# Optimization experiments

Hardware: AMD Instinct MI355X
Metric: run time of the kernel (lower is better)

Reference implementation:

```python
import jax, jax.numpy as jnp
import numpy as np

K = 512       # num_embeddings
D = 64        # dim_embeddings
BETA = 0.25   # commit_gain
GAMMA = 0.99  # EMA decay
EPS = 1e-05   # Laplace smoothing


def setup_inputs() -> dict:
    key = jax.random.key(0)
    k1, k2, k3 = jax.random.split(key, 3)
    enc_pred = jax.random.normal(k1, (32, D, 64, 64), dtype=jnp.float32)
    embeddings = jax.random.normal(k2, (K, D), dtype=jnp.float32)
    ema_m = jax.random.normal(k3, (K, D), dtype=jnp.float32)
    ema_M = jnp.zeros((K, 1), dtype=jnp.float32)
    return {"enc_pred": enc_pred, "embeddings": embeddings,
            "ema_m": ema_m, "ema_M": ema_M}


def reference(enc_pred, embeddings, ema_m, ema_M):
    B, _, H, W = enc_pred.shape
    x = jnp.transpose(enc_pred, (0, 2, 3, 1))          # [B, H, W, D]
    flat = x.reshape(-1, D)                            # [N, D], N = B*H*W

    # Squared L2 distances to all codewords: [N, K]
    dist = (jnp.sum(flat * flat, axis=1, keepdims=True)
            + jnp.sum(embeddings * embeddings, axis=1)
            - 2.0 * flat @ embeddings.T)
    idx = jnp.argmin(dist, axis=1)                     # [N]

    # Codebook lookup (equivalent to one-hot @ embeddings)
    quantized = embeddings[idx].reshape(x.shape)       # [B, H, W, D]

    # EMA codebook update (training branch, no_grad in torch)
    dm = jax.ops.segment_sum(flat, idx, num_segments=K)                 # [K, D]
    counts = jax.ops.segment_sum(jnp.ones((flat.shape[0], 1), flat.dtype),
                                 idx, num_segments=K)                   # [K, 1]
    new_m = GAMMA * ema_m + (1.0 - GAMMA) * dm
    new_M = GAMMA * ema_M + (1.0 - GAMMA) * counts
    N_tot = jnp.sum(new_M)
    new_M = (new_M + EPS) / (N_tot + EPS * K) * N_tot
    new_embeddings = new_m / new_M

    # Commitment loss (quantized detached)
    loss = BETA * jnp.mean((jax.lax.stop_gradient(quantized) - x) ** 2)

    # Straight-through estimator
    quant_ste = x + jax.lax.stop_gradient(quantized - x)
    out = jnp.transpose(quant_ste, (0, 3, 1, 2))       # [B, D, H, W]

    idx_ret = idx.reshape(B, H, W)[:, None, :, :]      # [B, 1, H, W]
    return (out, loss, idx_ret, new_embeddings, new_m, new_M)
```

## Files before the change

### kernel.cpp

```cpp
#include <hip/hip_runtime.h>

#define KCODES 512
#define DIM 64
#define NB 32
#define NH 64
#define NW 64
#define NPTS (NB*NH*NW)
#define HW (NH*NW)

#define O_OUT  0
#define O_LOSS 8388608
#define O_IDX  8388609
#define O_EMB  8519681
#define O_M    8552449
#define O_MM   8585217

#define W_DM   0
#define W_CNT  (KCODES*DIM)
#define W_LOSS (W_CNT + KCODES)
#define W_NEWM (W_LOSS + 1)
#define W_C    (W_NEWM + KCODES)
#define W_TOTAL (W_C + KCODES)

#define XPAD 68
#define EPAD 68

__global__ void cnorm_kernel(const float* __restrict__ emb, float* __restrict__ ws) {
    int k = blockIdx.x * blockDim.x + threadIdx.x;
    if (k >= KCODES) return;
    float s = 0.f;
    #pragma unroll
    for (int d = 0; d < DIM; ++d) { float v = emb[k*DIM + d]; s += v*v; }
    ws[W_C + k] = s;
}

__global__ __launch_bounds__(256, 2) void assign_kernel(
    const float* __restrict__ enc, const float* __restrict__ emb,
    float* __restrict__ out, float* __restrict__ ws)
{
    __shared__ float XL[128*XPAD];
    __shared__ float EL[128*EPAD];
    __shared__ float cnT[128];
    __shared__ int   bestI[128];

    const int t  = threadIdx.x;
    const int tx = t & 15;
    const int ty = t >> 4;
    const int wv = t >> 6, w = t & 63;
    const int R0 = blockIdx.x * 2;

    #pragma unroll
    for (int r2 = 0; r2 < 2; ++r2) {
        int R = R0 + r2, b = R >> 6, h = R & 63;
        const float* base = enc + (size_t)b*64*HW + (size_t)h*64 + w;
        int p = r2*64 + w;
        #pragma unroll
        for (int it = 0; it < 4; ++it) {
            int d0 = (it*4 + wv)*4;
            float4 v = make_float4(base[(size_t)(d0+0)*HW], base[(size_t)(d0+1)*HW],
                                   base[(size_t)(d0+2)*HW], base[(size_t)(d0+3)*HW]);
            *(float4*)(&XL[p*XPAD + d0]) = v;
        }
    }

    float best[8]; int bidx[8];
    #pragma unroll
    for (int i = 0; i < 8; ++i) { best[i] = 3.402823466e38f; bidx[i] = 0; }

    for (int tile = 0; tile < 4; ++tile) {
        __syncthreads();
        const float* esrc = emb + (size_t)tile*128*64;
        #pragma unroll
        for (int it = 0; it < 8; ++it) {
            int idx = t + it*256;
            *(float4*)(&EL[(idx >> 4)*EPAD + (idx & 15)*4]) =
                *(const float4*)(esrc + (idx >> 4)*64 + (idx & 15)*4);
        }
        if (t < 128) cnT[t] = ws[W_C + tile*128 + t];
        __syncthreads();

        float acc[8][8];
        #pragma unroll
        for (int i = 0; i < 8; ++i)
            #pragma unroll
            for (int j = 0; j < 8; ++j) acc[i][j] = 0.f;

        for (int c = 0; c < 16; ++c) {
            float4 xf[8], ef[8];
            #pragma unroll
            for (int i = 0; i < 8; ++i) {
                int p = 2*ty + (i&1) + 32*(i>>1);
                xf[i] = *(const float4*)(&XL[p*XPAD + c*4]);
            }
            #pragma unroll
            for (int j = 0; j < 8; ++j) {
                int r = tx + 16*j;
                ef[j] = *(const float4*)(&EL[r*EPAD + c*4]);
            }
            #pragma unroll
            for (int i = 0; i < 8; ++i)
                #pragma unroll
                for (int j = 0; j < 8; ++j) {
                    acc[i][j] = fmaf(xf[i].x, ef[j].x, acc[i][j]);
                    acc[i][j] = fmaf(xf[i].y, ef[j].y, acc[i][j]);
                    acc[i][j] = fmaf(xf[i].z, ef[j].z, acc[i][j]);
                    acc[i][j] = fmaf(xf[i].w, ef[j].w, acc[i][j]);
                }
        }

        #pragma unroll
        for (int j = 0; j < 8; ++j) {
            int k = tile*128 + tx + 16*j;
            float cn = cnT[tx + 16*j];
            #pragma unroll
            for (int i = 0; i < 8; ++i) {
                float s = cn - 2.f*acc[i][j];
                if (s < best[i] || (s == best[i] && k < bidx[i])) { best[i] = s; bidx[i] = k; }
            }
        }
    }

    #pragma unroll
    for (int i = 0; i < 8; ++i) {
        float b = best[i]; int kx = bidx[i];
        #pragma unroll
        for (int off = 1; off < 16; off <<= 1) {
            float ob = __shfl_xor(b, off, 64);
            int   ok = __shfl_xor(kx, off, 64);
            if (ob < b || (ob == b && ok < kx)) { b = ob; kx = ok; }
        }
        if (tx == 0) bestI[2*ty + (i&1) + 32*(i>>1)] = kx;
    }
    __syncthreads();
    if (t < 128) out[O_IDX + (size_t)R0*64 + t] = (float)bestI[t];
}

__global__ __launch_bounds__(512, 1) void scatter_kernel(
    const float* __restrict__ enc, const float* __restrict__ emb,
    float* __restrict__ out, float* __restrict__ ws)
{
    __shared__ float dmL[KCODES][DIM+1];
    __shared__ float cntL[KCODES];
    __shared__ float redL[8];

    const int t  = threadIdx.x;
    const int w  = t & 63;
    const int wv = t >> 6;
    const int pg = w >> 4, dl = w & 15;

    float* dmf = &dmL[0][0];
    for (int i = t; i < KCODES*(DIM+1); i += 512) dmf[i] = 0.f;
    if (t < KCODES) cntL[t] = 0.f;
    __syncthreads();

    const int R = blockIdx.x * 8 + wv;
    const int b = R >> 6, h = R & 63;
    const float* base  = enc + (size_t)b*(64*HW) + (size_t)h*64;
    float*       obase = out + O_OUT + (size_t)b*(64*HW) + (size_t)h*64;

    const int bidx = (int)out[O_IDX + (size_t)R*64 + w];
    atomicAdd(&cntL[bidx], 1.0f);
    float lsum = 0.f;

    #pragma unroll
    for (int c = 0; c < 4; ++c) {
        #pragma unroll
        for (int jj = 0; jj < 16; ++jj) {
            int p  = jj*4 + pg;
            int kb = __shfl(bidx, p, 64);
            int d  = c*16 + dl;
            float xv = base[(size_t)d*HW + p];
            atomicAdd(&dmL[kb][d], xv);
            float q = emb[kb*64 + d];
            obase[(size_t)d*HW + p] = q;
            float df = q - xv;
            lsum = fmaf(df, df, lsum);
        }
    }

    #pragma unroll
    for (int off = 32; off >= 1; off >>= 1) lsum += __shfl_down(lsum, off, 64);
    if (w == 0) redL[wv] = lsum;
    __syncthreads();
    if (t == 0) {
        float s = 0.f;
        #pragma unroll
        for (int v = 0; v < 8; ++v) s += redL[v];
        atomicAdd(&ws[W_LOSS], s);
    }

    for (int k = wv*64; k < wv*64 + 64; ++k) {
        float c = cntL[k];
        if (c == 0.f) continue;
        atomicAdd(&ws[W_DM + k*64 + w], dmL[k][w]);
        if (w == 0) atomicAdd(&ws[W_CNT + k], c);
    }
}

__global__ void finalizeA(const float* __restrict__ emaM,
                          float* __restrict__ out, float* __restrict__ ws)
{
    __shared__ float red[512];
    int k = threadIdx.x;
    float nM = 0.99f * emaM[k] + 0.01f * ws[W_CNT + k];
    red[k] = nM;
    __syncthreads();
    for (int s = 256; s >= 1; s >>= 1) {
        if (k < s) red[k] += red[k + s];
        __syncthreads();
    }
    float Ntot = red[0];
    float sm = (nM + 1e-5f) / (Ntot + 1e-5f * (float)KCODES) * Ntot;
    ws[W_NEWM + k] = sm;
    out[O_MM + k] = sm;
    if (k == 0) out[O_LOSS] = 0.25f * ws[W_LOSS] / (float)((size_t)NPTS * DIM);
}

__global__ void finalizeB(const float* __restrict__ emam,
                          float* __restrict__ out, const float* __restrict__ ws)
{
    int i = blockIdx.x * blockDim.x + threadIdx.x;
    int k = i >> 6;
    float nm = 0.99f * emam[i] + 0.01f * ws[W_DM + i];
    out[O_M + i] = nm;
    out[O_EMB + i] = nm / ws[W_NEWM + k];
}

extern "C" void kernel_launch(void* const* d_in, const int* in_sizes, int n_in,
                              void* d_out, int out_size, void* d_ws, size_t ws_size,
                              hipStream_t stream)
{
    const float* enc  = (const float*)d_in[0];
    const float* emb  = (const float*)d_in[1];
    const float* emam = (const float*)d_in[2];
    const float* emaM = (const float*)d_in[3];
    float* out = (float*)d_out;
    float* ws  = (float*)d_ws;

    hipMemsetAsync(ws, 0, (size_t)W_TOTAL * sizeof(float), stream);
    cnorm_kernel<<<2, 256, 0, stream>>>(emb, ws);
    assign_kernel<<<NPTS/128, 256, 0, stream>>>(enc, emb, out, ws);
    scatter_kernel<<<256, 512, 0, stream>>>(enc, emb, out, ws);
    finalizeA<<<1, 512, 0, stream>>>(emaM, out, ws);
    finalizeB<<<(KCODES*DIM)/256, 256, 0, stream>>>(emam, out, ws);
}
```

Baseline: 243.5 us.

## Use split-bf16 MFMA for distance GEMM with exact fp32 fallback on near ties

The assign kernel's FP32 FMA distance computation is replaced by bf16 MFMA instructions, with each operand split into a high and a low bf16 part and three cross products summed to approximate FP32 accuracy. The kernel tracks the best and second-best distance per point. Points whose gap is below a fixed threshold are recomputed exactly in FP32 against all codes, so the argmin still matches the reference. This removes the scalar-FMA compute bound but adds per-element bf16 conversion work and a serial fallback loop with block-wide syncs.

```diff
diff --git a/kernel.cpp b/kernel.cpp
--- a/kernel.cpp
+++ b/kernel.cpp
@@ -22,8 +22,19 @@
 #define W_C    (W_NEWM + KCODES)
 #define W_TOTAL (W_C + KCODES)
 
-#define XPAD 68
-#define EPAD 68
+#define XSTR 72
+#define EPS_GAP 0.0625f
+
+using bfrag = __attribute__((ext_vector_type(8))) short;
+using f32x4 = __attribute__((ext_vector_type(4))) float;
+
+__device__ __forceinline__ unsigned short f2bh(float x) {
+    unsigned u = __float_as_uint(x);
+    return (unsigned short)((u + 0x7FFFu + ((u >> 16) & 1u)) >> 16);
+}
+__device__ __forceinline__ float bf2f(unsigned short h) {
+    return __uint_as_float(((unsigned)h) << 16);
+}
 
 __global__ void cnorm_kernel(const float* __restrict__ emb, float* __restrict__ ws) {
     int k = blockIdx.x * blockDim.x + threadIdx.x;
@@ -38,34 +49,55 @@
     const float* __restrict__ enc, const float* __restrict__ emb,
     float* __restrict__ out, float* __restrict__ ws)
 {
-    __shared__ float XL[128*XPAD];
-    __shared__ float EL[128*EPAD];
+    __shared__ unsigned short XH[128*XSTR], XLo[128*XSTR];
+    __shared__ unsigned short EH[128*XSTR], ELo[128*XSTR];
     __shared__ float cnT[128];
     __shared__ int   bestI[128];
+    __shared__ float gapL[128];
+    __shared__ float rsS[4]; __shared__ int rsK[4];
 
     const int t  = threadIdx.x;
-    const int tx = t & 15;
-    const int ty = t >> 4;
-    const int wv = t >> 6, w = t & 63;
+    const int l  = t & 63;
+    const int wv = t >> 6;
     const int R0 = blockIdx.x * 2;
 
     #pragma unroll
     for (int r2 = 0; r2 < 2; ++r2) {
         int R = R0 + r2, b = R >> 6, h = R & 63;
-        const float* base = enc + (size_t)b*64*HW + (size_t)h*64 + w;
-        int p = r2*64 + w;
+        const float* base = enc + (size_t)b*64*HW + (size_t)h*64 + (t & 63);
+        int p = r2*64 + (t & 63);
         #pragma unroll
         for (int it = 0; it < 4; ++it) {
             int d0 = (it*4 + wv)*4;
             float4 v = make_float4(base[(size_t)(d0+0)*HW], base[(size_t)(d0+1)*HW],
                                    base[(size_t)(d0+2)*HW], base[(size_t)(d0+3)*HW]);
-            *(float4*)(&XL[p*XPAD + d0]) = v;
-        }
-    }
-
-    float best[8]; int bidx[8];
-    #pragma unroll
-    for (int i = 0; i < 8; ++i) { best[i] = 3.402823466e38f; bidx[i] = 0; }
+            unsigned short h0=f2bh(v.x), h1=f2bh(v.y), h2=f2bh(v.z), h3=f2bh(v.w);
+            float4 lo = make_float4(v.x-bf2f(h0), v.y-bf2f(h1), v.z-bf2f(h2), v.w-bf2f(h3));
+            unsigned short g0=f2bh(lo.x), g1=f2bh(lo.y), g2=f2bh(lo.z), g3=f2bh(lo.w);
+            *(uint2*)&XH [p*XSTR + d0] = make_uint2((unsigned)h0|((unsigned)h1<<16),
+                                                    (unsigned)h2|((unsigned)h3<<16));
+            *(uint2*)&XLo[p*XSTR + d0] = make_uint2((unsigned)g0|((unsigned)g1<<16),
+                                                    (unsigned)g2|((unsigned)g3<<16));
+        }
+    }
+    __syncthreads();
+
+    const int row16 = l & 15, kgrp = l >> 4;
+    const int mtA = wv*2, mtB = wv*2 + 1;
+    bfrag ah00 = *(bfrag*)&XH [(mtA*16+row16)*XSTR +  0 + kgrp*8];
+    bfrag ah01 = *(bfrag*)&XH [(mtA*16+row16)*XSTR + 32 + kgrp*8];
+    bfrag ah10 = *(bfrag*)&XH [(mtB*16+row16)*XSTR +  0 + kgrp*8];
+    bfrag ah11 = *(bfrag*)&XH [(mtB*16+row16)*XSTR + 32 + kgrp*8];
+    bfrag al00 = *(bfrag*)&XLo[(mtA*16+row16)*XSTR +  0 + kgrp*8];
+    bfrag al01 = *(bfrag*)&XLo[(mtA*16+row16)*XSTR + 32 + kgrp*8];
+    bfrag al10 = *(bfrag*)&XLo[(mtB*16+row16)*XSTR +  0 + kgrp*8];
+    bfrag al11 = *(bfrag*)&XLo[(mtB*16+row16)*XSTR + 32 + kgrp*8];
+
+    float b1[2][4], b2[2][4]; int k1[2][4];
+    #pragma unroll
+    for (int mi = 0; mi < 2; ++mi)
+        #pragma unroll
+        for (int r = 0; r < 4; ++r) { b1[mi][r] = 3.402823466e38f; b2[mi][r] = 3.402823466e38f; k1[mi][r] = 0; }
 
     for (int tile = 0; tile < 4; ++tile) {
         __syncthreads();
@@ -73,65 +105,116 @@
         #pragma unroll
         for (int it = 0; it < 8; ++it) {
             int idx = t + it*256;
-            *(float4*)(&EL[(idx >> 4)*EPAD + (idx & 15)*4]) =
-                *(const float4*)(esrc + (idx >> 4)*64 + (idx & 15)*4);
+            int er = idx >> 4, ec = (idx & 15)*4;
+            float4 v = *(const float4*)(esrc + er*64 + ec);
+            unsigned short h0=f2bh(v.x), h1=f2bh(v.y), h2=f2bh(v.z), h3=f2bh(v.w);
+            float4 lo = make_float4(v.x-bf2f(h0), v.y-bf2f(h1), v.z-bf2f(h2), v.w-bf2f(h3));
+            unsigned short g0=f2bh(lo.x), g1=f2bh(lo.y), g2=f2bh(lo.z), g3=f2bh(lo.w);
+            *(uint2*)&EH [er*XSTR + ec] = make_uint2((unsigned)h0|((unsigned)h1<<16),
+                                                     (unsigned)h2|((unsigned)h3<<16));
+            *(uint2*)&ELo[er*XSTR + ec] = make_uint2((unsigned)g0|((unsigned)g1<<16),
+                                                     (unsigned)g2|((unsigned)g3<<16));
         }
         if (t < 128) cnT[t] = ws[W_C + tile*128 + t];
         __syncthreads();
 
-        float acc[8][8];
-        #pragma unroll
-        for (int i = 0; i < 8; ++i)
+        for (int nt = 0; nt < 8; ++nt) {
+            bfrag bh0 = *(bfrag*)&EH [(nt*16+row16)*XSTR +  0 + kgrp*8];
+            bfrag bh1 = *(bfrag*)&EH [(nt*16+row16)*XSTR + 32 + kgrp*8];
+            bfrag bl0 = *(bfrag*)&ELo[(nt*16+row16)*XSTR +  0 + kgrp*8];
+            bfrag bl1 = *(bfrag*)&ELo[(nt*16+row16)*XSTR + 32 + kgrp*8];
+            float cnv = cnT[nt*16 + row16];
+            int kcol = tile*128 + nt*16 + row16;
+
+            f32x4 acc = {0.f, 0.f, 0.f, 0.f};
+            acc = __builtin_amdgcn_mfma_f32_16x16x32_bf16(ah00, bh0, acc, 0,0,0);
+            acc = __builtin_amdgcn_mfma_f32_16x16x32_bf16(ah01, bh1, acc, 0,0,0);
+            acc = __builtin_amdgcn_mfma_f32_16x16x32_bf16(ah00, bl0, acc, 0,0,0);
+            acc = __builtin_amdgcn_mfma_f32_16x16x32_bf16(ah01, bl1, acc, 0,0,0);
+            acc = __builtin_amdgcn_mfma_f32_16x16x32_bf16(al00, bh0, acc, 0,0,0);
+            acc = __builtin_amdgcn_mfma_f32_16x16x32_bf16(al01, bh1, acc, 0,0,0);
             #pragma unroll
-            for (int j = 0; j < 8; ++j) acc[i][j] = 0.f;
-
-        for (int c = 0; c < 16; ++c) {
-            float4 xf[8], ef[8];
+            for (int r = 0; r < 4; ++r) {
+                float s = fmaf(-2.f, acc[r], cnv);
+                if (s < b1[0][r]) { b2[0][r] = b1[0][r]; b1[0][r] = s; k1[0][r] = kcol; }
+                else if (s < b2[0][r]) b2[0][r] = s;
+            }
+            f32x4 ac2 = {0.f, 0.f, 0.f, 0.f};
+            ac2 = __builtin_amdgcn_mfma_f32_16x16x32_bf16(ah10, bh0, ac2, 0,0,0);
+            ac2 = __builtin_amdgcn_mfma_f32_16x16x32_bf16(ah11, bh1, ac2, 0,0,0);
+            ac2 = __builtin_amdgcn_mfma_f32_16x16x32_bf16(ah10, bl0, ac2, 0,0,0);
+            ac2 = __builtin_amdgcn_mfma_f32_16x16x32_bf16(ah11, bl1, ac2, 0,0,0);
+            ac2 = __builtin_amdgcn_mfma_f32_16x16x32_bf16(al10, bh0, ac2, 0,0,0);
+            ac2 = __builtin_amdgcn_mfma_f32_16x16x32_bf16(al11, bh1, ac2, 0,0,0);
             #pragma unroll
-            for (int i = 0; i < 8; ++i) {
-                int p = 2*ty + (i&1) + 32*(i>>1);
-                xf[i] = *(const float4*)(&XL[p*XPAD + c*4]);
+            for (int r = 0; r < 4; ++r) {
+                float s = fmaf(-2.f, ac2[r], cnv);
+                if (s < b1[1][r]) { b2[1][r] = b1[1][r]; b1[1][r] = s; k1[1][r] = kcol; }
+                else if (s < b2[1][r]) b2[1][r] = s;
             }
+        }
+    }
+
+    #pragma unroll
+    for (int mi = 0; mi < 2; ++mi)
+        #pragma unroll
+        for (int r = 0; r < 4; ++r) {
+            float b = b1[mi][r], c2 = b2[mi][r]; int kk = k1[mi][r];
             #pragma unroll
-            for (int j = 0; j < 8; ++j) {
-                int r = tx + 16*j;
-                ef[j] = *(const float4*)(&EL[r*EPAD + c*4]);
+            for (int off = 1; off < 16; off <<= 1) {
+                float ob  = __shfl_xor(b,  off, 64);
+                int   ok  = __shfl_xor(kk, off, 64);
+                float oc2 = __shfl_xor(c2, off, 64);
+                bool win = (ob < b) || (ob == b && ok < kk);
+                if (win) { c2 = fminf(b, oc2); b = ob; kk = ok; }
+                else     { c2 = fminf(c2, ob); }
             }
+            if (row16 == 0) {
+                int p = (wv*2 + mi)*16 + kgrp*4 + r;
+                bestI[p] = kk; gapL[p] = c2 - b;
+            }
+        }
+    __syncthreads();
+
+    for (int p = 0; p < 128; ++p) {
+        if (gapL[p] >= EPS_GAP) continue;
+        const int P = R0*64 + p;
+        const float* xb = enc + ((size_t)(P >> 12))*(64*HW)
+                              + ((size_t)((P >> 6) & 63))*64 + (P & 63);
+        const float* e0 = emb + t*64;
+        const float* e1 = emb + (t+256)*64;
+        float dot0 = 0.f, dot1 = 0.f;
+        #pragma unroll
+        for (int d4 = 0; d4 < 16; ++d4) {
+            float4 ev0 = *(const float4*)(e0 + d4*4);
+            float4 ev1 = *(const float4*)(e1 + d4*4);
+            float x0 = xb[(size_t)(d4*4+0)*HW], x1 = xb[(size_t)(d4*4+1)*HW];
+            float x2 = xb[(size_t)(d4*4+2)*HW], x3 = xb[(size_t)(d4*4+3)*HW];
+            dot0 = fmaf(x0,ev0.x,fmaf(x1,ev0.y,fmaf(x2,ev0.z,fmaf(x3,ev0.w,dot0))));
+            dot1 = fmaf(x0,ev1.x,fmaf(x1,ev1.y,fmaf(x2,ev1.z,fmaf(x3,ev1.w,dot1))));
+        }
+        float s0 = ws[W_C + t]       - 2.f*dot0;
+        float s1 = ws[W_C + t + 256] - 2.f*dot1;
+        float sb; int kb;
+        if (s0 <= s1) { sb = s0; kb = t; } else { sb = s1; kb = t + 256; }
+        #pragma unroll
+        for (int off = 1; off < 64; off <<= 1) {
+            float ob = __shfl_xor(sb, off, 64);
+            int   ok = __shfl_xor(kb, off, 64);
+            if (ob < sb || (ob == sb && ok < kb)) { sb = ob; kb = ok; }
+        }
+        if (l == 0) { rsS[wv] = sb; rsK[wv] = kb; }
+        __syncthreads();
+        if (t == 0) {
+            float bb = rsS[0]; int bk = rsK[0];
             #pragma unroll
-            for (int i = 0; i < 8; ++i)
-                #pragma unroll
-                for (int j = 0; j < 8; ++j) {
-                    acc[i][j] = fmaf(xf[i].x, ef[j].x, acc[i][j]);
-                    acc[i][j] = fmaf(xf[i].y, ef[j].y, acc[i][j]);
-                    acc[i][j] = fmaf(xf[i].z, ef[j].z, acc[i][j]);
-                    acc[i][j] = fmaf(xf[i].w, ef[j].w, acc[i][j]);
-                }
-        }
-
-        #pragma unroll
-        for (int j = 0; j < 8; ++j) {
-            int k = tile*128 + tx + 16*j;
-            float cn = cnT[tx + 16*j];
-            #pragma unroll
-            for (int i = 0; i < 8; ++i) {
-                float s = cn - 2.f*acc[i][j];
-                if (s < best[i] || (s == best[i] && k < bidx[i])) { best[i] = s; bidx[i] = k; }
-            }
-        }
-    }
-
-    #pragma unroll
-    for (int i = 0; i < 8; ++i) {
-        float b = best[i]; int kx = bidx[i];
-        #pragma unroll
-        for (int off = 1; off < 16; off <<= 1) {
-            float ob = __shfl_xor(b, off, 64);
-            int   ok = __shfl_xor(kx, off, 64);
-            if (ob < b || (ob == b && ok < kx)) { b = ob; kx = ok; }
-        }
-        if (tx == 0) bestI[2*ty + (i&1) + 32*(i>>1)] = kx;
-    }
-    __syncthreads();
+            for (int v = 1; v < 4; ++v)
+                if (rsS[v] < bb || (rsS[v] == bb && rsK[v] < bk)) { bb = rsS[v]; bk = rsK[v]; }
+            bestI[p] = bk;
+        }
+        __syncthreads();
+    }
+
     if (t < 128) out[O_IDX + (size_t)R0*64 + t] = (float)bestI[t];
 }
 
```

Measured after the change: 246.9 us. No clear change (+1.4%).

## Compute codebook distances with split-bf16 MFMA and exact fp32 tie rescoring

Applied to the files above, without the earlier changes.

Replaces the fp32 FMA distance GEMM in the assignment kernel with bf16 MFMA instructions. Both operands are split into high and low bf16 parts (three products) to approximate fp32 accuracy. A new prep kernel pre-packs the codebook into MFMA fragment layout in the workspace. The kernel tracks the best and second-best distance per point, and points whose gap falls below a threshold are rescored exactly in fp32 to keep argmin results matching the reference. The risk is extra prep work and divergent rescoring cost if many points are flagged.

```diff
diff --git a/kernel.cpp b/kernel.cpp
--- a/kernel.cpp
+++ b/kernel.cpp
@@ -20,10 +20,30 @@
 #define W_LOSS (W_CNT + KCODES)
 #define W_NEWM (W_LOSS + 1)
 #define W_C    (W_NEWM + KCODES)
-#define W_TOTAL (W_C + KCODES)
-
-#define XPAD 68
-#define EPAD 68
+#define W_EHF  34308
+#define W_ELF  (W_EHF + 16384)
+#define W_TOTAL (W_ELF + 16384)
+
+#define EPS_GAP 0.0625f
+
+using bfrag = __attribute__((ext_vector_type(8))) short;
+using f32x4 = __attribute__((ext_vector_type(4))) float;
+
+__device__ __forceinline__ unsigned short f2bh(float x) {
+    unsigned u = __float_as_uint(x);
+    return (unsigned short)((u + 0x7FFFu + ((u >> 16) & 1u)) >> 16);
+}
+__device__ __forceinline__ float bf2f(unsigned short h) {
+    return __uint_as_float(((unsigned)h) << 16);
+}
+__device__ __forceinline__ unsigned fmap(float s) {
+    unsigned b = __float_as_uint(s);
+    return b ^ (unsigned)(((int)b >> 31) | (int)0x80000000);
+}
+__device__ __forceinline__ float finv(unsigned u) {
+    unsigned b = (u & 0x80000000u) ? (u ^ 0x80000000u) : ~u;
+    return __uint_as_float(b);
+}
 
 __global__ void cnorm_kernel(const float* __restrict__ emb, float* __restrict__ ws) {
     int k = blockIdx.x * blockDim.x + threadIdx.x;
@@ -34,104 +54,175 @@
     ws[W_C + k] = s;
 }
 
-__global__ __launch_bounds__(256, 2) void assign_kernel(
+__global__ void prep_kernel(const float* __restrict__ emb, float* __restrict__ ws) {
+    int tid = blockIdx.x * 256 + threadIdx.x;
+    int k = tid >> 3, g = tid & 7;
+    int h = g >> 2, kg = g & 3;
+    int lane = kg*16 + (k & 15);
+    int d0 = h*32 + kg*8;
+    size_t dst = ((size_t)((k >> 4)*2 + h)*64 + lane)*8;
+    unsigned hi[4], lo[4];
+    #pragma unroll
+    for (int jp = 0; jp < 4; ++jp) {
+        float x0 = emb[k*64 + d0 + 2*jp], x1 = emb[k*64 + d0 + 2*jp + 1];
+        unsigned short h0 = f2bh(x0), h1 = f2bh(x1);
+        unsigned short l0 = f2bh(x0 - bf2f(h0)), l1 = f2bh(x1 - bf2f(h1));
+        hi[jp] = (unsigned)h0 | ((unsigned)h1 << 16);
+        lo[jp] = (unsigned)l0 | ((unsigned)l1 << 16);
+    }
+    unsigned short* EHF = (unsigned short*)(ws + W_EHF);
+    unsigned short* ELF = (unsigned short*)(ws + W_ELF);
+    *(uint4*)&EHF[dst] = make_uint4(hi[0], hi[1], hi[2], hi[3]);
+    *(uint4*)&ELF[dst] = make_uint4(lo[0], lo[1], lo[2], lo[3]);
+}
+
+__global__ __launch_bounds__(256, 3) void assign_kernel(
     const float* __restrict__ enc, const float* __restrict__ emb,
-    float* __restrict__ out, float* __restrict__ ws)
-{
-    __shared__ float XL[128*XPAD];
-    __shared__ float EL[128*EPAD];
-    __shared__ float cnT[128];
-    __shared__ int   bestI[128];
+    const float* __restrict__ ws, float* __restrict__ out)
+{
+    __shared__ float XL[128*68];
+    __shared__ int bestI[128];
+    __shared__ int flagP[128];
+    __shared__ int nflag;
 
     const int t  = threadIdx.x;
-    const int tx = t & 15;
-    const int ty = t >> 4;
-    const int wv = t >> 6, w = t & 63;
+    const int lw = t & 63;
+    const int wv = t >> 6;
+    const int row16 = lw & 15, kgrp = lw >> 4;
     const int R0 = blockIdx.x * 2;
+
+    if (t == 0) nflag = 0;
 
     #pragma unroll
     for (int r2 = 0; r2 < 2; ++r2) {
         int R = R0 + r2, b = R >> 6, h = R & 63;
-        const float* base = enc + (size_t)b*64*HW + (size_t)h*64 + w;
-        int p = r2*64 + w;
+        const float* base = enc + (size_t)b*64*HW + (size_t)h*64 + lw;
+        int p = r2*64 + lw;
         #pragma unroll
         for (int it = 0; it < 4; ++it) {
             int d0 = (it*4 + wv)*4;
             float4 v = make_float4(base[(size_t)(d0+0)*HW], base[(size_t)(d0+1)*HW],
                                    base[(size_t)(d0+2)*HW], base[(size_t)(d0+3)*HW]);
-            *(float4*)(&XL[p*XPAD + d0]) = v;
-        }
-    }
-
-    float best[8]; int bidx[8];
-    #pragma unroll
-    for (int i = 0; i < 8; ++i) { best[i] = 3.402823466e38f; bidx[i] = 0; }
-
-    for (int tile = 0; tile < 4; ++tile) {
-        __syncthreads();
-        const float* esrc = emb + (size_t)tile*128*64;
-        #pragma unroll
-        for (int it = 0; it < 8; ++it) {
-            int idx = t + it*256;
-            *(float4*)(&EL[(idx >> 4)*EPAD + (idx & 15)*4]) =
-                *(const float4*)(esrc + (idx >> 4)*64 + (idx & 15)*4);
-        }
-        if (t < 128) cnT[t] = ws[W_C + tile*128 + t];
-        __syncthreads();
-
-        float acc[8][8];
-        #pragma unroll
-        for (int i = 0; i < 8; ++i)
+            *(float4*)(&XL[p*68 + d0]) = v;
+        }
+    }
+    __syncthreads();
+
+    bfrag ah[2][2], al[2][2];
+    #pragma unroll
+    for (int mi = 0; mi < 2; ++mi) {
+        int Mt = wv*2 + mi;
+        #pragma unroll
+        for (int hf = 0; hf < 2; ++hf) {
+            const float* src = &XL[(Mt*16 + row16)*68 + hf*32 + kgrp*8];
+            float4 f0 = *(const float4*)(src);
+            float4 f1 = *(const float4*)(src + 4);
+            unsigned short h0=f2bh(f0.x),h1=f2bh(f0.y),h2=f2bh(f0.z),h3=f2bh(f0.w);
+            unsigned short h4=f2bh(f1.x),h5=f2bh(f1.y),h6=f2bh(f1.z),h7=f2bh(f1.w);
+            ah[mi][hf] = (bfrag){(short)h0,(short)h1,(short)h2,(short)h3,
+                                 (short)h4,(short)h5,(short)h6,(short)h7};
+            al[mi][hf] = (bfrag){(short)f2bh(f0.x-bf2f(h0)),(short)f2bh(f0.y-bf2f(h1)),
+                                 (short)f2bh(f0.z-bf2f(h2)),(short)f2bh(f0.w-bf2f(h3)),
+                                 (short)f2bh(f1.x-bf2f(h4)),(short)f2bh(f1.y-bf2f(h5)),
+                                 (short)f2bh(f1.z-bf2f(h6)),(short)f2bh(f1.w-bf2f(h7))};
+        }
+    }
+
+    const unsigned short* EHF = (const unsigned short*)(ws + W_EHF);
+    const unsigned short* ELF = (const unsigned short*)(ws + W_ELF);
+    const float* cns = ws + W_C;
+
+    unsigned u1[2][4], u2[2][4]; int k1[2][4];
+    #pragma unroll
+    for (int mi = 0; mi < 2; ++mi)
+        #pragma unroll
+        for (int r = 0; r < 4; ++r) { u1[mi][r] = 0xFFFFFFFFu; u2[mi][r] = 0xFFFFFFFFu; k1[mi][r] = 0; }
+
+    #pragma unroll 2
+    for (int t8 = 0; t8 < 32; ++t8) {
+        bfrag bh0 = *(const bfrag*)&EHF[((size_t)(t8*2+0)*64 + lw)*8];
+        bfrag bh1 = *(const bfrag*)&EHF[((size_t)(t8*2+1)*64 + lw)*8];
+        bfrag bl0 = *(const bfrag*)&ELF[((size_t)(t8*2+0)*64 + lw)*8];
+        bfrag bl1 = *(const bfrag*)&ELF[((size_t)(t8*2+1)*64 + lw)*8];
+        float cnv = cns[t8*16 + row16];
+        int  kcol = t8*16 + row16;
+        #pragma unroll
+        for (int mi = 0; mi < 2; ++mi) {
+            f32x4 acc = {0.f, 0.f, 0.f, 0.f};
+            acc = __builtin_amdgcn_mfma_f32_16x16x32_bf16(ah[mi][0], bh0, acc, 0,0,0);
+            acc = __builtin_amdgcn_mfma_f32_16x16x32_bf16(ah[mi][1], bh1, acc, 0,0,0);
+            acc = __builtin_amdgcn_mfma_f32_16x16x32_bf16(ah[mi][0], bl0, acc, 0,0,0);
+            acc = __builtin_amdgcn_mfma_f32_16x16x32_bf16(ah[mi][1], bl1, acc, 0,0,0);
+            acc = __builtin_amdgcn_mfma_f32_16x16x32_bf16(al[mi][0], bh0, acc, 0,0,0);
+            acc = __builtin_amdgcn_mfma_f32_16x16x32_bf16(al[mi][1], bh1, acc, 0,0,0);
             #pragma unroll
-            for (int j = 0; j < 8; ++j) acc[i][j] = 0.f;
-
-        for (int c = 0; c < 16; ++c) {
-            float4 xf[8], ef[8];
+            for (int r = 0; r < 4; ++r) {
+                float s = fmaf(-2.f, acc[r], cnv);
+                unsigned u = fmap(s);
+                bool win = u < u1[mi][r];
+                u2[mi][r] = win ? u1[mi][r] : (u < u2[mi][r] ? u : u2[mi][r]);
+                k1[mi][r] = win ? kcol : k1[mi][r];
+                u1[mi][r] = win ? u : u1[mi][r];
+            }
+        }
+    }
+
+    #pragma unroll
+    for (int mi = 0; mi < 2; ++mi)
+        #pragma unroll
+        for (int r = 0; r < 4; ++r) {
+            unsigned long long v = ((unsigned long long)u1[mi][r] << 32) | (unsigned)k1[mi][r];
+            unsigned c2 = u2[mi][r];
             #pragma unroll
-            for (int i = 0; i < 8; ++i) {
-                int p = 2*ty + (i&1) + 32*(i>>1);
-                xf[i] = *(const float4*)(&XL[p*XPAD + c*4]);
+            for (int off = 1; off < 16; off <<= 1) {
+                unsigned long long ov = __shfl_xor(v, off, 64);
+                unsigned oc2 = __shfl_xor(c2, off, 64);
+                unsigned ob = (unsigned)(ov >> 32), mb = (unsigned)(v >> 32);
+                bool win = ov < v;
+                c2 = win ? (mb < oc2 ? mb : oc2) : (c2 < ob ? c2 : ob);
+                v  = win ? ov : v;
             }
+            if (row16 == 0) {
+                int p = (wv*2 + mi)*16 + kgrp*4 + r;
+                bestI[p] = (int)(unsigned)v;
+                float gap = finv(c2) - finv((unsigned)(v >> 32));
+                if (gap < EPS_GAP) { int pos = atomicAdd(&nflag, 1); flagP[pos] = p; }
+            }
+        }
+    __syncthreads();
+
+    int nf = nflag;
+    for (int f = wv; f < nf; f += 4) {
+        int p = flagP[f];
+        float dot[8];
+        #pragma unroll
+        for (int c = 0; c < 8; ++c) dot[c] = 0.f;
+        const float* er = emb + (size_t)(lw*8)*64;
+        for (int d4 = 0; d4 < 16; ++d4) {
+            float4 xv = *(const float4*)(&XL[p*68 + d4*4]);
             #pragma unroll
-            for (int j = 0; j < 8; ++j) {
-                int r = tx + 16*j;
-                ef[j] = *(const float4*)(&EL[r*EPAD + c*4]);
+            for (int c = 0; c < 8; ++c) {
+                float4 ev = *(const float4*)(er + c*64 + d4*4);
+                dot[c] = fmaf(xv.x, ev.x, fmaf(xv.y, ev.y,
+                         fmaf(xv.z, ev.z, fmaf(xv.w, ev.w, dot[c]))));
             }
-            #pragma unroll
-            for (int i = 0; i < 8; ++i)
-                #pragma unroll
-                for (int j = 0; j < 8; ++j) {
-                    acc[i][j] = fmaf(xf[i].x, ef[j].x, acc[i][j]);
-                    acc[i][j] = fmaf(xf[i].y, ef[j].y, acc[i][j]);
-                    acc[i][j] = fmaf(xf[i].z, ef[j].z, acc[i][j]);
-                    acc[i][j] = fmaf(xf[i].w, ef[j].w, acc[i][j]);
-                }
-        }
-
-        #pragma unroll
-        for (int j = 0; j < 8; ++j) {
-            int k = tile*128 + tx + 16*j;
-            float cn = cnT[tx + 16*j];
-            #pragma unroll
-            for (int i = 0; i < 8; ++i) {
-                float s = cn - 2.f*acc[i][j];
-                if (s < best[i] || (s == best[i] && k < bidx[i])) { best[i] = s; bidx[i] = k; }
-            }
-        }
-    }
-
-    #pragma unroll
-    for (int i = 0; i < 8; ++i) {
-        float b = best[i]; int kx = bidx[i];
-        #pragma unroll
-        for (int off = 1; off < 16; off <<= 1) {
-            float ob = __shfl_xor(b, off, 64);
-            int   ok = __shfl_xor(kx, off, 64);
-            if (ob < b || (ob == b && ok < kx)) { b = ob; kx = ok; }
-        }
-        if (tx == 0) bestI[2*ty + (i&1) + 32*(i>>1)] = kx;
-    }
-    __syncthreads();
+        }
+        unsigned long long vb = 0xFFFFFFFFFFFFFFFFull;
+        #pragma unroll
+        for (int c = 0; c < 8; ++c) {
+            float s = cns[lw*8 + c] - 2.f*dot[c];
+            unsigned long long vv = ((unsigned long long)fmap(s) << 32) | (unsigned)(lw*8 + c);
+            vb = (vv < vb) ? vv : vb;
+        }
+        #pragma unroll
+        for (int off = 1; off < 64; off <<= 1) {
+            unsigned long long ov = __shfl_xor(vb, off, 64);
+            vb = (ov < vb) ? ov : vb;
+        }
+        if (lw == 0) bestI[p] = (int)(unsigned)vb;
+    }
+    __syncthreads();
+
     if (t < 128) out[O_IDX + (size_t)R0*64 + t] = (float)bestI[t];
 }
 
@@ -237,9 +328,10 @@
     float* out = (float*)d_out;
     float* ws  = (float*)d_ws;
 
-    hipMemsetAsync(ws, 0, (size_t)W_TOTAL * sizeof(float), stream);
+    hipMemsetAsync(ws, 0, (size_t)33794 * sizeof(float), stream);
     cnorm_kernel<<<2, 256, 0, stream>>>(emb, ws);
-    assign_kernel<<<NPTS/128, 256, 0, stream>>>(enc, emb, out, ws);
+    prep_kernel<<<16, 256, 0, stream>>>(emb, ws);
+    assign_kernel<<<NPTS/128, 256, 0, stream>>>(enc, emb, ws, out);
     scatter_kernel<<<256, 512, 0, stream>>>(enc, emb, out, ws);
     finalizeA<<<1, 512, 0, stream>>>(emaM, out, ws);
     finalizeB<<<(KCODES*DIM)/256, 256, 0, stream>>>(emam, out, ws);
```

Result: slower. 315.7 us (+29.6%).

## Split scatter into atomic and output wave roles; fuse finalize kernels

Applied to the files above, without the earlier changes.

The scatter kernel now launches 1024 threads per block. Half the waves do the shared-memory atomic accumulation of codeword sums and counts. The other half write the quantized output and accumulate the loss, so the two memory streams can overlap. The two finalize kernels become one elementwise kernel: the total of the new EMA counts is computed algebraically from the sum of ema_M (reduced in cnorm) plus the known point count. This removes the single-block reduction launch, at the cost of each thread recomputing the smoothed count and both roles reloading the input.

```diff
diff --git a/kernel.cpp b/kernel.cpp
--- a/kernel.cpp
+++ b/kernel.cpp
@@ -16,22 +16,28 @@
 #define O_MM   8585217
 
 #define W_DM   0
-#define W_CNT  (KCODES*DIM)
-#define W_LOSS (W_CNT + KCODES)
-#define W_NEWM (W_LOSS + 1)
-#define W_C    (W_NEWM + KCODES)
-#define W_TOTAL (W_C + KCODES)
+#define W_CNT  32768
+#define W_LOSS 33280
+#define W_SUMM 33281
+#define W_C    33282
+#define W_ZERO 33282
 
 #define XPAD 68
 #define EPAD 68
 
-__global__ void cnorm_kernel(const float* __restrict__ emb, float* __restrict__ ws) {
+__global__ void cnorm_kernel(const float* __restrict__ emb,
+                             const float* __restrict__ emaM,
+                             float* __restrict__ ws) {
     int k = blockIdx.x * blockDim.x + threadIdx.x;
     if (k >= KCODES) return;
     float s = 0.f;
     #pragma unroll
     for (int d = 0; d < DIM; ++d) { float v = emb[k*DIM + d]; s += v*v; }
     ws[W_C + k] = s;
+    float m = emaM[k];
+    #pragma unroll
+    for (int off = 32; off >= 1; off >>= 1) m += __shfl_down(m, off, 64);
+    if ((k & 63) == 0) atomicAdd(&ws[W_SUMM], m);
 }
 
 __global__ __launch_bounds__(256, 2) void assign_kernel(
@@ -135,46 +141,60 @@
     if (t < 128) out[O_IDX + (size_t)R0*64 + t] = (float)bestI[t];
 }
 
-__global__ __launch_bounds__(512, 1) void scatter_kernel(
+__global__ __launch_bounds__(1024, 1) void scatter_kernel(
     const float* __restrict__ enc, const float* __restrict__ emb,
     float* __restrict__ out, float* __restrict__ ws)
 {
     __shared__ float dmL[KCODES][DIM+1];
     __shared__ float cntL[KCODES];
-    __shared__ float redL[8];
+    __shared__ float redL[16];
 
     const int t  = threadIdx.x;
     const int w  = t & 63;
     const int wv = t >> 6;
+    const int rw = wv & 7;
+    const int role = wv >> 3;
     const int pg = w >> 4, dl = w & 15;
 
     float* dmf = &dmL[0][0];
-    for (int i = t; i < KCODES*(DIM+1); i += 512) dmf[i] = 0.f;
+    for (int i = t; i < KCODES*(DIM+1); i += 1024) dmf[i] = 0.f;
     if (t < KCODES) cntL[t] = 0.f;
     __syncthreads();
 
-    const int R = blockIdx.x * 8 + wv;
+    const int R = blockIdx.x * 8 + rw;
     const int b = R >> 6, h = R & 63;
     const float* base  = enc + (size_t)b*(64*HW) + (size_t)h*64;
     float*       obase = out + O_OUT + (size_t)b*(64*HW) + (size_t)h*64;
 
     const int bidx = (int)out[O_IDX + (size_t)R*64 + w];
-    atomicAdd(&cntL[bidx], 1.0f);
     float lsum = 0.f;
 
-    #pragma unroll
-    for (int c = 0; c < 4; ++c) {
-        #pragma unroll
-        for (int jj = 0; jj < 16; ++jj) {
-            int p  = jj*4 + pg;
-            int kb = __shfl(bidx, p, 64);
-            int d  = c*16 + dl;
-            float xv = base[(size_t)d*HW + p];
-            atomicAdd(&dmL[kb][d], xv);
-            float q = emb[kb*64 + d];
-            obase[(size_t)d*HW + p] = q;
-            float df = q - xv;
-            lsum = fmaf(df, df, lsum);
+    if (role == 0) {
+        atomicAdd(&cntL[bidx], 1.0f);
+        #pragma unroll
+        for (int c = 0; c < 4; ++c) {
+            #pragma unroll
+            for (int jj = 0; jj < 16; ++jj) {
+                int p  = jj*4 + pg;
+                int kb = __shfl(bidx, p, 64);
+                int d  = c*16 + dl;
+                atomicAdd(&dmL[kb][d], base[(size_t)d*HW + p]);
+            }
+        }
+    } else {
+        #pragma unroll
+        for (int c = 0; c < 4; ++c) {
+            #pragma unroll
+            for (int jj = 0; jj < 16; ++jj) {
+                int p  = jj*4 + pg;
+                int kb = __shfl(bidx, p, 64);
+                int d  = c*16 + dl;
+                float xv = base[(size_t)d*HW + p];
+                float q  = emb[kb*64 + d];
+                obase[(size_t)d*HW + p] = q;
+                float df = q - xv;
+                lsum = fmaf(df, df, lsum);
+            }
         }
     }
 
@@ -185,11 +205,11 @@
     if (t == 0) {
         float s = 0.f;
         #pragma unroll
-        for (int v = 0; v < 8; ++v) s += redL[v];
+        for (int v = 8; v < 16; ++v) s += redL[v];
         atomicAdd(&ws[W_LOSS], s);
     }
 
-    for (int k = wv*64; k < wv*64 + 64; ++k) {
+    for (int k = wv*32; k < wv*32 + 32; ++k) {
         float c = cntL[k];
         if (c == 0.f) continue;
         atomicAdd(&ws[W_DM + k*64 + w], dmL[k][w]);
@@ -197,33 +217,21 @@
     }
 }
 
-__global__ void finalizeA(const float* __restrict__ emaM,
-                          float* __restrict__ out, float* __restrict__ ws)
-{
-    __shared__ float red[512];
-    int k = threadIdx.x;
-    float nM = 0.99f * emaM[k] + 0.01f * ws[W_CNT + k];
-    red[k] = nM;
-    __syncthreads();
-    for (int s = 256; s >= 1; s >>= 1) {
-        if (k < s) red[k] += red[k + s];
-        __syncthreads();
-    }
-    float Ntot = red[0];
-    float sm = (nM + 1e-5f) / (Ntot + 1e-5f * (float)KCODES) * Ntot;
-    ws[W_NEWM + k] = sm;
-    out[O_MM + k] = sm;
-    if (k == 0) out[O_LOSS] = 0.25f * ws[W_LOSS] / (float)((size_t)NPTS * DIM);
-}
-
-__global__ void finalizeB(const float* __restrict__ emam,
-                          float* __restrict__ out, const float* __restrict__ ws)
+__global__ void finalize_kernel(const float* __restrict__ emam,
+                                const float* __restrict__ emaM,
+                                float* __restrict__ out,
+                                const float* __restrict__ ws)
 {
     int i = blockIdx.x * blockDim.x + threadIdx.x;
     int k = i >> 6;
+    float Ntot = 0.99f * ws[W_SUMM] + 0.01f * (float)NPTS;
+    float nM = 0.99f * emaM[k] + 0.01f * ws[W_CNT + k];
+    float sm = (nM + 1e-5f) / (Ntot + 1e-5f * (float)KCODES) * Ntot;
     float nm = 0.99f * emam[i] + 0.01f * ws[W_DM + i];
     out[O_M + i] = nm;
-    out[O_EMB + i] = nm / ws[W_NEWM + k];
+    out[O_EMB + i] = nm / sm;
+    if ((i & 63) == 0) out[O_MM + k] = sm;
+    if (i == 0) out[O_LOSS] = 0.25f * ws[W_LOSS] / (float)((size_t)NPTS * DIM);
 }
 
 extern "C" void kernel_launch(void* const* d_in, const int* in_sizes, int n_in,
@@ -237,10 +245,9 @@
     float* out = (float*)d_out;
     float* ws  = (float*)d_ws;
 
-    hipMemsetAsync(ws, 0, (size_t)W_TOTAL * sizeof(float), stream);
-    cnorm_kernel<<<2, 256, 0, stream>>>(emb, ws);
+    hipMemsetAsync(ws, 0, (size_t)W_ZERO * sizeof(float), stream);
+    cnorm_kernel<<<2, 256, 0, stream>>>(emb, emaM, ws);
     assign_kernel<<<NPTS/128, 256, 0, stream>>>(enc, emb, out, ws);
-    scatter_kernel<<<256, 512, 0, stream>>>(enc, emb, out, ws);
-    finalizeA<<<1, 512, 0, stream>>>(emaM, out, ws);
-    finalizeB<<<(KCODES*DIM)/256, 256, 0, stream>>>(emam, out, ws);
-}
+    scatter_kernel<<<256, 1024, 0, stream>>>(enc, emb, out, ws);
+    finalize_kernel<<<(KCODES*DIM)/256, 256, 0, stream>>>(emam, emaM, out, ws);
+}
```

New measurement: 238.3 us. 1.02x faster.
